# Kernel tuning notes

Hardware: AMD Instinct MI355X
Metric: run time of the kernel (lower is better)

Reference implementation:

```python
import jax, jax.numpy as jnp
import numpy as np

IN_FEAT, H_FEAT, NUM_CLASSES = 7, 8, 2
N_NODES, N_EDGES, N_GRAPHS = 40000, 640000, 64
DIMS = [IN_FEAT, H_FEAT, H_FEAT * 2, H_FEAT * 4, H_FEAT * 8, H_FEAT * 16]  # 7,8,16,32,64,128


def setup_inputs() -> dict:
    key = jax.random.key(0)
    ks = jax.random.split(key, 20)
    inp = {
        "x": jax.random.normal(ks[0], (N_NODES, IN_FEAT), dtype=jnp.float32),
        "edge_index": jax.random.randint(ks[1], (2, N_EDGES), 0, N_NODES, dtype=jnp.int32),
        "edge_attr": jax.random.uniform(ks[2], (N_EDGES,), dtype=jnp.float32),
        "batch": jnp.sort(jax.random.randint(ks[3], (N_NODES,), 0, N_GRAPHS, dtype=jnp.int32)),
    }
    # GraphConv params: lin_rel (with bias) applied to aggregated messages,
    # lin_root (no bias) applied to x itself. Stored as [in, out]; y = x @ W.
    for i in range(5):
        fi, fo = DIMS[i], DIMS[i + 1]
        s = 1.0 / np.sqrt(fi)
        inp[f"w_rel{i+1}"] = jax.random.uniform(ks[4 + 3 * i], (fi, fo), minval=-s, maxval=s, dtype=jnp.float32)
        inp[f"b_rel{i+1}"] = jax.random.uniform(ks[5 + 3 * i], (fo,), minval=-s, maxval=s, dtype=jnp.float32)
        inp[f"w_root{i+1}"] = jax.random.uniform(ks[6 + 3 * i], (fi, fo), minval=-s, maxval=s, dtype=jnp.float32)
    s = 1.0 / np.sqrt(DIMS[-1])
    inp["w_lin"] = jax.random.uniform(ks[19], (DIMS[-1], NUM_CLASSES), minval=-s, maxval=s, dtype=jnp.float32)
    inp["b_lin"] = jax.random.uniform(jax.random.fold_in(key, 99), (NUM_CLASSES,), minval=-s, maxval=s, dtype=jnp.float32)
    return inp


def graph_conv(x, src, dst, ew, w_rel, b_rel, w_root):
    # message: edge_weight * x[src]; aggregate by sum at dst (PyG GraphConv, aggr='add')
    msg = x[src] * ew[:, None]                               # [E, Fin]
    agg = jax.ops.segment_sum(msg, dst, num_segments=N_NODES)  # [N, Fin]
    return agg @ w_rel + b_rel + x @ w_root                  # [N, Fout]


def reference(x, edge_index, edge_attr, batch,
              w_rel1, b_rel1, w_root1, w_rel2, b_rel2, w_root2,
              w_rel3, b_rel3, w_root3, w_rel4, b_rel4, w_root4,
              w_rel5, b_rel5, w_root5, w_lin, b_lin):
    src, dst = edge_index[0], edge_index[1]
    h = x
    params = [(w_rel1, b_rel1, w_root1), (w_rel2, b_rel2, w_root2),
              (w_rel3, b_rel3, w_root3), (w_rel4, b_rel4, w_root4),
              (w_rel5, b_rel5, w_root5)]
    for wr, br, wo in params:
        h = graph_conv(h, src, dst, edge_attr, wr, br, wo)
    pooled = jax.ops.segment_sum(h, batch, num_segments=N_GRAPHS)  # [G, 128]
    return pooled @ w_lin + b_lin                                  # [G, 2]
```

## Files before the change

### kernel.cpp

```cpp
#include <hip/hip_runtime.h>

#define N_NODES 40000
#define N_EDGES 640000
#define N_GRAPHS 64

typedef unsigned short u16;
typedef unsigned int u32;
typedef __attribute__((ext_vector_type(8))) short bf16x8;
typedef __attribute__((ext_vector_type(4))) float f32x4;

static inline int cdiv(long long a, int b) { return (int)((a + b - 1) / b); }

__device__ __forceinline__ u16 f2bf(float f) {
    u32 u = __float_as_uint(f);
    u32 r = (u + 0x7fffu + ((u >> 16) & 1u)) >> 16;
    return (u16)r;
}
__device__ __forceinline__ u32 packpair(float a, float b) {
    return (u32)f2bf(a) | ((u32)f2bf(b) << 16);
}
__device__ __forceinline__ void unpack8(uint4 q, float* o) {
    o[0] = __uint_as_float(q.x << 16); o[1] = __uint_as_float(q.x & 0xffff0000u);
    o[2] = __uint_as_float(q.y << 16); o[3] = __uint_as_float(q.y & 0xffff0000u);
    o[4] = __uint_as_float(q.z << 16); o[5] = __uint_as_float(q.z & 0xffff0000u);
    o[6] = __uint_as_float(q.w << 16); o[7] = __uint_as_float(q.w & 0xffff0000u);
}

__device__ __forceinline__ void pack_one(int idx, int KS, int Kreal, int FOUT,
                                         const float* __restrict__ wrel,
                                         const float* __restrict__ wroot,
                                         u16* __restrict__ out) {
    int j = idx & 7;
    int lane = (idx >> 3) & 63;
    int rest = idx >> 9;
    int nt = rest / KS, ks = rest - nt * KS;
    int k = ks * 32 + (lane >> 4) * 8 + j;
    int col = nt * 16 + (lane & 15);
    float v = 0.f;
    if (k < Kreal / 2) v = wrel[k * FOUT + col];
    else if (k < Kreal) v = wroot[(k - Kreal / 2) * FOUT + col];
    out[idx] = f2bf(v);
}

__global__ __launch_bounds__(256) void prep_kernel(
        const float* __restrict__ x, u16* __restrict__ xbf,
        const float* __restrict__ wr2, const float* __restrict__ wo2,
        const float* __restrict__ wr3, const float* __restrict__ wo3,
        const float* __restrict__ wr4, const float* __restrict__ wo4,
        const float* __restrict__ wr5, const float* __restrict__ wo5,
        u16* __restrict__ p2, u16* __restrict__ p3,
        u16* __restrict__ p4, u16* __restrict__ p5,
        int* __restrict__ deg, float* __restrict__ pooled) {
    int tid = blockIdx.x * 256 + threadIdx.x;
    if (tid < 40000) {
        int n = tid;
        float v[8];
        #pragma unroll
        for (int i = 0; i < 7; ++i) v[i] = x[n * 7 + i];
        v[7] = 0.f;
        uint4 q;
        q.x = packpair(v[0], v[1]); q.y = packpair(v[2], v[3]);
        q.z = packpair(v[4], v[5]); q.w = packpair(v[6], v[7]);
        *(uint4*)(xbf + (long long)n * 8) = q;
    } else if (tid < 62016) {
        int t = tid - 40000;
        if (t < 512)        pack_one(t,        1,  16,  16,  wr2, wo2, p2);
        else if (t < 1536)  pack_one(t - 512,  1,  32,  32,  wr3, wo3, p3);
        else if (t < 5632)  pack_one(t - 1536, 2,  64,  64,  wr4, wo4, p4);
        else                pack_one(t - 5632, 4, 128, 128,  wr5, wo5, p5);
    } else if (tid < 102016) {
        deg[tid - 62016] = 0;
    } else if (tid < 110208) {
        pooled[tid - 102016] = 0.f;
    }
}

__global__ __launch_bounds__(256) void hist_kernel(const int* __restrict__ dst,
                                                   int* __restrict__ deg) {
    int e = blockIdx.x * 256 + threadIdx.x;
    if (e < N_EDGES) atomicAdd(&deg[dst[e]], 1);
}

__global__ __launch_bounds__(1024) void scan_part(const int* __restrict__ deg,
                                                  int* __restrict__ row_start,
                                                  int* __restrict__ bsum) {
    __shared__ int wtot[16], woff[16];
    int tid = threadIdx.x;
    int i = blockIdx.x * 1024 + tid;
    int v = (i < N_NODES) ? deg[i] : 0;
    int lane = tid & 63, wid = tid >> 6;
    int inc = v;
    #pragma unroll
    for (int off = 1; off < 64; off <<= 1) {
        int y = __shfl_up(inc, off, 64);
        if (lane >= off) inc += y;
    }
    if (lane == 63) wtot[wid] = inc;
    __syncthreads();
    if (tid < 16) {
        int b = wtot[tid];
        #pragma unroll
        for (int off = 1; off < 16; off <<= 1) {
            int y = __shfl_up(b, off, 16);
            if ((tid & 15) >= off) b += y;
        }
        woff[tid] = b - wtot[tid];
        if (tid == 15) bsum[blockIdx.x] = b;
    }
    __syncthreads();
    if (i <= N_NODES) row_start[i] = woff[wid] + inc - v;
}

__global__ __launch_bounds__(1024) void scan_add(int* __restrict__ row_start,
                                                 const int* __restrict__ bsum,
                                                 int* __restrict__ cursor) {
    __shared__ int sbase;
    int tid = threadIdx.x;
    if (tid < 64) {
        int b = (tid < blockIdx.x) ? bsum[tid] : 0;
        #pragma unroll
        for (int off = 32; off; off >>= 1) b += __shfl_xor(b, off, 64);
        if (tid == 0) sbase = b;
    }
    __syncthreads();
    int i = blockIdx.x * 1024 + tid;
    if (i <= N_NODES) {
        int v = row_start[i] + sbase;
        row_start[i] = v;
        if (i < N_NODES) cursor[i] = v;
    }
}

__global__ __launch_bounds__(256) void scatter_kernel(const int* __restrict__ src,
                                                      const int* __restrict__ dst,
                                                      const float* __restrict__ ew,
                                                      int* __restrict__ cursor,
                                                      int2* __restrict__ csr_pair) {
    int e = blockIdx.x * 256 + threadIdx.x;
    if (e >= N_EDGES) return;
    int pos = atomicAdd(&cursor[dst[e]], 1);
    int2 q;
    q.x = src[e];
    q.y = __float_as_int(ew[e]);
    csr_pair[pos] = q;
}

template<int LOGF, int SLOG>
__global__ __launch_bounds__(256) void gather_bf16(const u16* __restrict__ hin,
                                                   const int* __restrict__ rs,
                                                   const int2* __restrict__ pair,
                                                   u16* __restrict__ agg) {
    constexpr int FIN = 8 << LOGF;
    constexpr int S = 1 << SLOG;
    long long tid = (long long)blockIdx.x * 256 + threadIdx.x;
    int n = (int)(tid >> (LOGF + SLOG));
    if (n >= N_NODES) return;
    int sub = (int)(tid & ((1 << (LOGF + SLOG)) - 1));
    int c = sub & ((1 << LOGF) - 1);
    int half = sub >> LOGF;
    const u16* base = hin + c * 8;
    int beg = rs[n], end = rs[n + 1];
    float acc[8] = {0.f, 0.f, 0.f, 0.f, 0.f, 0.f, 0.f, 0.f};
    int p = beg + half;
    int s = 0; float w = 0.f;
    if (p < end) { int2 q = pair[p]; s = q.x; w = __int_as_float(q.y); }
    while (p < end) {
        uint4 rq = *(const uint4*)(base + (long long)s * FIN);
        float wc = w;
        int pn = p + S;
        if (pn < end) { int2 q = pair[pn]; s = q.x; w = __int_as_float(q.y); }
        float tv[8];
        unpack8(rq, tv);
        #pragma unroll
        for (int j = 0; j < 8; ++j) acc[j] = fmaf(wc, tv[j], acc[j]);
        p = pn;
    }
    #pragma unroll
    for (int d = (1 << LOGF); d < (1 << (LOGF + SLOG)); d <<= 1) {
        #pragma unroll
        for (int j = 0; j < 8; ++j) acc[j] += __shfl_xor(acc[j], d, 64);
    }
    if (half == 0) {
        uint4 o;
        o.x = packpair(acc[0], acc[1]); o.y = packpair(acc[2], acc[3]);
        o.z = packpair(acc[4], acc[5]); o.w = packpair(acc[6], acc[7]);
        *(uint4*)(agg + (long long)n * FIN + c * 8) = o;
    }
}

__global__ __launch_bounds__(256) void node1b(const u16* __restrict__ agg1,
                                              const u16* __restrict__ xbf,
                                              const float* __restrict__ wr,
                                              const float* __restrict__ br,
                                              const float* __restrict__ wo,
                                              u16* __restrict__ h2) {
    __shared__ float swr[56], swo[56], sb[8];
    if (threadIdx.x < 56) { swr[threadIdx.x] = wr[threadIdx.x]; swo[threadIdx.x] = wo[threadIdx.x]; }
    if (threadIdx.x < 8) sb[threadIdx.x] = br[threadIdx.x];
    __syncthreads();
    int n = blockIdx.x * 256 + threadIdx.x;
    if (n >= N_NODES) return;
    float a[8], h[8];
    uint4 qa = *(const uint4*)(agg1 + (long long)n * 8);
    uint4 qh = *(const uint4*)(xbf + (long long)n * 8);
    unpack8(qa, a);
    unpack8(qh, h);
    float o[8];
    #pragma unroll
    for (int j = 0; j < 8; ++j) {
        float s = sb[j];
        #pragma unroll
        for (int i = 0; i < 7; ++i) s = fmaf(a[i], swr[i * 8 + j], fmaf(h[i], swo[i * 8 + j], s));
        o[j] = s;
    }
    uint4 q;
    q.x = packpair(o[0], o[1]); q.y = packpair(o[2], o[3]);
    q.z = packpair(o[4], o[5]); q.w = packpair(o[6], o[7]);
    *(uint4*)(h2 + (long long)n * 8) = q;
}

template<int FIN, int FOUT, bool POOL>
__global__ __launch_bounds__(64) void node_mfma(const u16* __restrict__ agg,
                                                const u16* __restrict__ hin,
                                                const u16* __restrict__ bpack,
                                                const float* __restrict__ b_rel,
                                                u16* __restrict__ hout,
                                                const int* __restrict__ batch,
                                                float* __restrict__ pooled) {
    constexpr int KREAL = 2 * FIN;
    constexpr int K = (KREAL < 32) ? 32 : KREAL;
    constexpr int KS = K / 32;
    constexpr int NT = FOUT / 16;
    int lane = threadIdx.x;
    int tile = blockIdx.x;
    int col = lane & 15;
    int node_a = tile * 16 + col;
    int kgrp = (lane >> 4) * 8;

    f32x4 acc[NT];
    #pragma unroll
    for (int nt = 0; nt < NT; ++nt) {
        float bv = b_rel[nt * 16 + col];
        acc[nt] = (f32x4){bv, bv, bv, bv};
    }

    #pragma unroll
    for (int ks = 0; ks < KS; ++ks) {
        int k0 = ks * 32 + kgrp;
        bf16x8 af;
        if (k0 < FIN)
            af = *(const bf16x8*)(agg + (long long)node_a * FIN + k0);
        else if (k0 < KREAL)
            af = *(const bf16x8*)(hin + (long long)node_a * FIN + (k0 - FIN));
        else
            af = (bf16x8)(short)0;
        #pragma unroll
        for (int nt = 0; nt < NT; ++nt) {
            bf16x8 bf = *(const bf16x8*)(bpack + (((nt * KS + ks) << 6) + lane) * 8);
            acc[nt] = __builtin_amdgcn_mfma_f32_16x16x32_bf16(af, bf, acc[nt], 0, 0, 0);
        }
    }

    int row0 = tile * 16 + (lane >> 4) * 4;
    if constexpr (!POOL) {
        #pragma unroll
        for (int nt = 0; nt < NT; ++nt)
            #pragma unroll
            for (int r = 0; r < 4; ++r)
                hout[(long long)(row0 + r) * FOUT + nt * 16 + col] = f2bf(acc[nt][r]);
    } else {
        int b_first = batch[tile * 16];
        int b_last = batch[tile * 16 + 15];
        if (b_first == b_last) {
            #pragma unroll
            for (int nt = 0; nt < NT; ++nt) {
                float s = acc[nt][0] + acc[nt][1] + acc[nt][2] + acc[nt][3];
                s += __shfl_xor(s, 16, 64);
                s += __shfl_xor(s, 32, 64);
                if (lane < 16) atomicAdd(&pooled[b_first * FOUT + nt * 16 + col], s);
            }
        } else {
            #pragma unroll
            for (int r = 0; r < 4; ++r) {
                int g = batch[row0 + r];
                #pragma unroll
                for (int nt = 0; nt < NT; ++nt)
                    atomicAdd(&pooled[g * FOUT + nt * 16 + col], acc[nt][r]);
            }
        }
    }
}

__global__ void final_kernel(const float* __restrict__ pooled,
                             const float* __restrict__ w_lin,
                             const float* __restrict__ b_lin,
                             float* __restrict__ out) {
    int tid = threadIdx.x;
    int g = tid >> 1;
    int c = tid & 1;
    float acc = b_lin[c];
    #pragma unroll 8
    for (int fi = 0; fi < 128; ++fi)
        acc += pooled[g * 128 + fi] * w_lin[fi * 2 + c];
    out[g * 2 + c] = acc;
}

extern "C" void kernel_launch(void* const* d_in, const int* in_sizes, int n_in,
                              void* d_out, int out_size, void* d_ws, size_t ws_size,
                              hipStream_t stream) {
    const float* x     = (const float*)d_in[0];
    const int*   ei    = (const int*)d_in[1];
    const float* ea    = (const float*)d_in[2];
    const int*   batch = (const int*)d_in[3];
    const int* src = ei;
    const int* dst = ei + N_EDGES;

    const float* w_rel[5], *b_rel[5], *w_root[5];
    for (int i = 0; i < 5; ++i) {
        w_rel[i]  = (const float*)d_in[4 + 3 * i];
        b_rel[i]  = (const float*)d_in[5 + 3 * i];
        w_root[i] = (const float*)d_in[6 + 3 * i];
    }
    const float* w_lin = (const float*)d_in[19];
    const float* b_lin = (const float*)d_in[20];
    float* out = (float*)d_out;

    u16*   xbf     = (u16*)d_ws;
    u16*   agg     = xbf + 320000;
    u16*   h2      = agg + 2560000;
    u16*   h3      = h2 + 320000;
    u16*   h4      = h3 + 640000;
    u16*   h5      = h4 + 1280000;
    float* pooled  = (float*)(h5 + 2560000);
    u16*   p2      = (u16*)(pooled + N_GRAPHS * 128);
    u16*   p3      = p2 + 512;
    u16*   p4      = p3 + 1024;
    u16*   p5      = p4 + 4096;
    int2*  csr_pair= (int2*)(p5 + 16384);
    int*   deg     = (int*)(csr_pair + N_EDGES);
    int*   rs      = deg + N_NODES;
    int*   cursor  = rs + N_NODES + 1;
    int*   bsum    = cursor + N_NODES;

    const int BLK = 256;
    const int EB = cdiv(N_EDGES, BLK);

    prep_kernel<<<431, BLK, 0, stream>>>(x, xbf,
                                         w_rel[1], w_root[1], w_rel[2], w_root[2],
                                         w_rel[3], w_root[3], w_rel[4], w_root[4],
                                         p2, p3, p4, p5, deg, pooled);
    hist_kernel<<<EB, BLK, 0, stream>>>(dst, deg);
    scan_part<<<40, 1024, 0, stream>>>(deg, rs, bsum);
    scan_add<<<40, 1024, 0, stream>>>(rs, bsum, cursor);
    scatter_kernel<<<EB, BLK, 0, stream>>>(src, dst, ea, cursor, csr_pair);

    gather_bf16<0, 3><<<cdiv((long long)N_NODES * 8, BLK), BLK, 0, stream>>>(
        xbf, rs, csr_pair, agg);
    node1b<<<cdiv(N_NODES, BLK), BLK, 0, stream>>>(agg, xbf, w_rel[0], b_rel[0], w_root[0], h2);

    gather_bf16<0, 3><<<cdiv((long long)N_NODES * 8, BLK), BLK, 0, stream>>>(
        h2, rs, csr_pair, agg);
    node_mfma<8, 16, false><<<2500, 64, 0, stream>>>(agg, h2, p2, b_rel[1], h3, nullptr, nullptr);

    gather_bf16<1, 3><<<cdiv((long long)N_NODES * 16, BLK), BLK, 0, stream>>>(
        h3, rs, csr_pair, agg);
    node_mfma<16, 32, false><<<2500, 64, 0, stream>>>(agg, h3, p3, b_rel[2], h4, nullptr, nullptr);

    gather_bf16<2, 3><<<cdiv((long long)N_NODES * 32, BLK), BLK, 0, stream>>>(
        h4, rs, csr_pair, agg);
    node_mfma<32, 64, false><<<2500, 64, 0, stream>>>(agg, h4, p4, b_rel[3], h5, nullptr, nullptr);

    gather_bf16<3, 3><<<cdiv((long long)N_NODES * 64, BLK), BLK, 0, stream>>>(
        h5, rs, csr_pair, agg);
    node_mfma<64, 128, true><<<2500, 64, 0, stream>>>(agg, h5, p5, b_rel[4], nullptr, batch, pooled);

    final_kernel<<<1, 128, 0, stream>>>(pooled, w_lin, b_lin, out);
}
```

Measured before the change: 240.8 us.

## Fuse layer-1 gather with node transform, widen gather split, two tiles per MFMA block

Merges the first-layer edge gather and the 7->8 node transform into one kernel, so the intermediate aggregate never goes through global memory and one launch is removed. Raises the edge-split factor from 8 to 16 lanes per node for layers 2-4, giving more parallelism per node at the cost of extra shuffle reduction. Changes the MFMA node kernel so each 64-thread block handles two 16-node tiles, reusing the loaded weight fragments and halving the block count.

```diff
diff --git a/kernel.cpp b/kernel.cpp
--- a/kernel.cpp
+++ b/kernel.cpp
@@ -143,6 +143,52 @@
     q.x = src[e];
     q.y = __float_as_int(ew[e]);
     csr_pair[pos] = q;
+}
+
+__global__ __launch_bounds__(256) void gather_node1(const u16* __restrict__ xbf,
+                                                    const int* __restrict__ rs,
+                                                    const int2* __restrict__ pair,
+                                                    const float* __restrict__ wr,
+                                                    const float* __restrict__ br,
+                                                    const float* __restrict__ wo,
+                                                    u16* __restrict__ h2) {
+    __shared__ float swr[56], swo[56], sb[8];
+    if (threadIdx.x < 56) { swr[threadIdx.x] = wr[threadIdx.x]; swo[threadIdx.x] = wo[threadIdx.x]; }
+    if (threadIdx.x < 8) sb[threadIdx.x] = br[threadIdx.x];
+    __syncthreads();
+    int tid = blockIdx.x * 256 + threadIdx.x;
+    int n = tid >> 3;
+    if (n >= N_NODES) return;
+    int s3 = tid & 7;
+    int beg = rs[n], end = rs[n + 1];
+    float acc[8] = {0.f, 0.f, 0.f, 0.f, 0.f, 0.f, 0.f, 0.f};
+    int p = beg + s3;
+    int s = 0; float w = 0.f;
+    if (p < end) { int2 q = pair[p]; s = q.x; w = __int_as_float(q.y); }
+    while (p < end) {
+        uint4 rq = *(const uint4*)(xbf + (long long)s * 8);
+        float wc = w;
+        int pn = p + 8;
+        if (pn < end) { int2 q = pair[pn]; s = q.x; w = __int_as_float(q.y); }
+        float tv[8];
+        unpack8(rq, tv);
+        #pragma unroll
+        for (int j = 0; j < 8; ++j) acc[j] = fmaf(wc, tv[j], acc[j]);
+        p = pn;
+    }
+    #pragma unroll
+    for (int d = 1; d < 8; d <<= 1) {
+        #pragma unroll
+        for (int j = 0; j < 8; ++j) acc[j] += __shfl_xor(acc[j], d, 64);
+    }
+    uint4 qh = *(const uint4*)(xbf + (long long)n * 8);
+    float h[8];
+    unpack8(qh, h);
+    float o = sb[s3];
+    #pragma unroll
+    for (int i = 0; i < 7; ++i)
+        o = fmaf(acc[i], swr[i * 8 + s3], fmaf(h[i], swo[i * 8 + s3], o));
+    h2[(long long)n * 8 + s3] = f2bf(o);
 }
 
 template<int LOGF, int SLOG>
@@ -188,104 +234,87 @@
     }
 }
 
-__global__ __launch_bounds__(256) void node1b(const u16* __restrict__ agg1,
-                                              const u16* __restrict__ xbf,
-                                              const float* __restrict__ wr,
-                                              const float* __restrict__ br,
-                                              const float* __restrict__ wo,
-                                              u16* __restrict__ h2) {
-    __shared__ float swr[56], swo[56], sb[8];
-    if (threadIdx.x < 56) { swr[threadIdx.x] = wr[threadIdx.x]; swo[threadIdx.x] = wo[threadIdx.x]; }
-    if (threadIdx.x < 8) sb[threadIdx.x] = br[threadIdx.x];
-    __syncthreads();
-    int n = blockIdx.x * 256 + threadIdx.x;
-    if (n >= N_NODES) return;
-    float a[8], h[8];
-    uint4 qa = *(const uint4*)(agg1 + (long long)n * 8);
-    uint4 qh = *(const uint4*)(xbf + (long long)n * 8);
-    unpack8(qa, a);
-    unpack8(qh, h);
-    float o[8];
-    #pragma unroll
-    for (int j = 0; j < 8; ++j) {
-        float s = sb[j];
-        #pragma unroll
-        for (int i = 0; i < 7; ++i) s = fmaf(a[i], swr[i * 8 + j], fmaf(h[i], swo[i * 8 + j], s));
-        o[j] = s;
-    }
-    uint4 q;
-    q.x = packpair(o[0], o[1]); q.y = packpair(o[2], o[3]);
-    q.z = packpair(o[4], o[5]); q.w = packpair(o[6], o[7]);
-    *(uint4*)(h2 + (long long)n * 8) = q;
-}
-
 template<int FIN, int FOUT, bool POOL>
-__global__ __launch_bounds__(64) void node_mfma(const u16* __restrict__ agg,
-                                                const u16* __restrict__ hin,
-                                                const u16* __restrict__ bpack,
-                                                const float* __restrict__ b_rel,
-                                                u16* __restrict__ hout,
-                                                const int* __restrict__ batch,
-                                                float* __restrict__ pooled) {
+__global__ __launch_bounds__(64) void node_mfma2(const u16* __restrict__ agg,
+                                                 const u16* __restrict__ hin,
+                                                 const u16* __restrict__ bpack,
+                                                 const float* __restrict__ b_rel,
+                                                 u16* __restrict__ hout,
+                                                 const int* __restrict__ batch,
+                                                 float* __restrict__ pooled) {
     constexpr int KREAL = 2 * FIN;
     constexpr int K = (KREAL < 32) ? 32 : KREAL;
     constexpr int KS = K / 32;
     constexpr int NT = FOUT / 16;
     int lane = threadIdx.x;
-    int tile = blockIdx.x;
+    int tp = blockIdx.x * 2;
     int col = lane & 15;
-    int node_a = tile * 16 + col;
     int kgrp = (lane >> 4) * 8;
-
-    f32x4 acc[NT];
+    long long nA0 = (long long)(tp * 16 + col) * FIN;
+    long long nA1 = nA0 + 16LL * FIN;
+
+    f32x4 acc0[NT], acc1[NT];
     #pragma unroll
     for (int nt = 0; nt < NT; ++nt) {
         float bv = b_rel[nt * 16 + col];
-        acc[nt] = (f32x4){bv, bv, bv, bv};
+        acc0[nt] = (f32x4){bv, bv, bv, bv};
+        acc1[nt] = (f32x4){bv, bv, bv, bv};
     }
 
     #pragma unroll
     for (int ks = 0; ks < KS; ++ks) {
         int k0 = ks * 32 + kgrp;
-        bf16x8 af;
-        if (k0 < FIN)
-            af = *(const bf16x8*)(agg + (long long)node_a * FIN + k0);
-        else if (k0 < KREAL)
-            af = *(const bf16x8*)(hin + (long long)node_a * FIN + (k0 - FIN));
-        else
-            af = (bf16x8)(short)0;
+        bf16x8 af0, af1;
+        if (k0 < FIN) {
+            af0 = *(const bf16x8*)(agg + nA0 + k0);
+            af1 = *(const bf16x8*)(agg + nA1 + k0);
+        } else if (k0 < KREAL) {
+            af0 = *(const bf16x8*)(hin + nA0 + (k0 - FIN));
+            af1 = *(const bf16x8*)(hin + nA1 + (k0 - FIN));
+        } else {
+            af0 = (bf16x8)(short)0;
+            af1 = (bf16x8)(short)0;
+        }
         #pragma unroll
         for (int nt = 0; nt < NT; ++nt) {
             bf16x8 bf = *(const bf16x8*)(bpack + (((nt * KS + ks) << 6) + lane) * 8);
-            acc[nt] = __builtin_amdgcn_mfma_f32_16x16x32_bf16(af, bf, acc[nt], 0, 0, 0);
+            acc0[nt] = __builtin_amdgcn_mfma_f32_16x16x32_bf16(af0, bf, acc0[nt], 0, 0, 0);
+            acc1[nt] = __builtin_amdgcn_mfma_f32_16x16x32_bf16(af1, bf, acc1[nt], 0, 0, 0);
         }
     }
 
-    int row0 = tile * 16 + (lane >> 4) * 4;
+    int lrow = (lane >> 4) * 4;
     if constexpr (!POOL) {
         #pragma unroll
         for (int nt = 0; nt < NT; ++nt)
             #pragma unroll
-            for (int r = 0; r < 4; ++r)
-                hout[(long long)(row0 + r) * FOUT + nt * 16 + col] = f2bf(acc[nt][r]);
+            for (int r = 0; r < 4; ++r) {
+                hout[(long long)(tp * 16 + lrow + r) * FOUT + nt * 16 + col] = f2bf(acc0[nt][r]);
+                hout[(long long)(tp * 16 + 16 + lrow + r) * FOUT + nt * 16 + col] = f2bf(acc1[nt][r]);
+            }
     } else {
-        int b_first = batch[tile * 16];
-        int b_last = batch[tile * 16 + 15];
-        if (b_first == b_last) {
-            #pragma unroll
-            for (int nt = 0; nt < NT; ++nt) {
-                float s = acc[nt][0] + acc[nt][1] + acc[nt][2] + acc[nt][3];
-                s += __shfl_xor(s, 16, 64);
-                s += __shfl_xor(s, 32, 64);
-                if (lane < 16) atomicAdd(&pooled[b_first * FOUT + nt * 16 + col], s);
-            }
-        } else {
-            #pragma unroll
-            for (int r = 0; r < 4; ++r) {
-                int g = batch[row0 + r];
+        #pragma unroll
+        for (int t = 0; t < 2; ++t) {
+            f32x4* acc = t ? acc1 : acc0;
+            int base = (tp + t) * 16;
+            int b_first = batch[base];
+            int b_last = batch[base + 15];
+            if (b_first == b_last) {
                 #pragma unroll
-                for (int nt = 0; nt < NT; ++nt)
-                    atomicAdd(&pooled[g * FOUT + nt * 16 + col], acc[nt][r]);
+                for (int nt = 0; nt < NT; ++nt) {
+                    float s = acc[nt][0] + acc[nt][1] + acc[nt][2] + acc[nt][3];
+                    s += __shfl_xor(s, 16, 64);
+                    s += __shfl_xor(s, 32, 64);
+                    if (lane < 16) atomicAdd(&pooled[b_first * FOUT + nt * 16 + col], s);
+                }
+            } else {
+                #pragma unroll
+                for (int r = 0; r < 4; ++r) {
+                    int g = batch[base + lrow + r];
+                    #pragma unroll
+                    for (int nt = 0; nt < NT; ++nt)
+                        atomicAdd(&pooled[g * FOUT + nt * 16 + col], acc[nt][r]);
+                }
             }
         }
     }
@@ -354,25 +383,23 @@
     scan_add<<<40, 1024, 0, stream>>>(rs, bsum, cursor);
     scatter_kernel<<<EB, BLK, 0, stream>>>(src, dst, ea, cursor, csr_pair);
 
-    gather_bf16<0, 3><<<cdiv((long long)N_NODES * 8, BLK), BLK, 0, stream>>>(
-        xbf, rs, csr_pair, agg);
-    node1b<<<cdiv(N_NODES, BLK), BLK, 0, stream>>>(agg, xbf, w_rel[0], b_rel[0], w_root[0], h2);
-
-    gather_bf16<0, 3><<<cdiv((long long)N_NODES * 8, BLK), BLK, 0, stream>>>(
+    gather_node1<<<1250, BLK, 0, stream>>>(xbf, rs, csr_pair, w_rel[0], b_rel[0], w_root[0], h2);
+
+    gather_bf16<0, 4><<<cdiv((long long)N_NODES * 16, BLK), BLK, 0, stream>>>(
         h2, rs, csr_pair, agg);
-    node_mfma<8, 16, false><<<2500, 64, 0, stream>>>(agg, h2, p2, b_rel[1], h3, nullptr, nullptr);
-
-    gather_bf16<1, 3><<<cdiv((long long)N_NODES * 16, BLK), BLK, 0, stream>>>(
+    node_mfma2<8, 16, false><<<1250, 64, 0, stream>>>(agg, h2, p2, b_rel[1], h3, nullptr, nullptr);
+
+    gather_bf16<1, 4><<<cdiv((long long)N_NODES * 32, BLK), BLK, 0, stream>>>(
         h3, rs, csr_pair, agg);
-    node_mfma<16, 32, false><<<2500, 64, 0, stream>>>(agg, h3, p3, b_rel[2], h4, nullptr, nullptr);
-
-    gather_bf16<2, 3><<<cdiv((long long)N_NODES * 32, BLK), BLK, 0, stream>>>(
+    node_mfma2<16, 32, false><<<1250, 64, 0, stream>>>(agg, h3, p3, b_rel[2], h4, nullptr, nullptr);
+
+    gather_bf16<2, 4><<<cdiv((long long)N_NODES * 64, BLK), BLK, 0, stream>>>(
         h4, rs, csr_pair, agg);
-    node_mfma<32, 64, false><<<2500, 64, 0, stream>>>(agg, h4, p4, b_rel[3], h5, nullptr, nullptr);
+    node_mfma2<32, 64, false><<<1250, 64, 0, stream>>>(agg, h4, p4, b_rel[3], h5, nullptr, nullptr);
 
     gather_bf16<3, 3><<<cdiv((long long)N_NODES * 64, BLK), BLK, 0, stream>>>(
         h5, rs, csr_pair, agg);
-    node_mfma<64, 128, true><<<2500, 64, 0, stream>>>(agg, h5, p5, b_rel[4], nullptr, batch, pooled);
+    node_mfma2<64, 128, true><<<1250, 64, 0, stream>>>(agg, h5, p5, b_rel[4], nullptr, batch, pooled);
 
     final_kernel<<<1, 128, 0, stream>>>(pooled, w_lin, b_lin, out);
 }
```

Measured after the change: 247.4 us. 2.7% more time.
